# Kernel tuning notes

Measured on AMD Instinct MI355X. Metric: run time of the kernel, lower is better.

Reference implementation:

```python
import jax, jax.numpy as jnp
import numpy as np

NUM_BINS = 16


def _luma(x):
    # x: [B, 3, H, W] -> [B, H, W]
    return 0.299 * x[:, 0] + 0.587 * x[:, 1] + 0.114 * x[:, 2]


def setup_inputs() -> dict:
    key = jax.random.key(0)
    k1, k2, k3 = jax.random.split(key, 3)
    shape = (16, 3, 512, 512)
    pred = jax.random.uniform(k1, shape, dtype=jnp.float32)
    target = jax.random.uniform(k2, shape, dtype=jnp.float32)
    input_img = jax.random.uniform(k3, shape, dtype=jnp.float32)
    return {"pred": pred, "target": target, "input_img": input_img}


def reference(pred, target, input_img):
    nb = NUM_BINS
    pl = _luma(pred).ravel()
    tl = _luma(target).ravel()
    il = _luma(input_img).ravel()
    # bin i covers [i/nb, (i+1)/nb); values >= 1.0 fall in NO bin in the
    # original loop, so route them to an extra segment that is discarded.
    bins = jnp.clip(jnp.floor(il * nb).astype(jnp.int32), 0, nb - 1)
    bins = jnp.where(il >= 1.0, nb, bins)
    ones = jnp.ones_like(il)
    counts = jax.ops.segment_sum(ones, bins, num_segments=nb + 1)[:nb]
    psum = jax.ops.segment_sum(pl, bins, num_segments=nb + 1)[:nb]
    tsum = jax.ops.segment_sum(tl, bins, num_segments=nb + 1)[:nb]
    safe = jnp.maximum(counts, 1.0)
    per_bin = jnp.where(counts > 0, jnp.abs(psum / safe - tsum / safe), 0.0)
    return jnp.sum(per_bin) / nb
```

## Files before the change

### kernel.cpp

```cpp
#include <hip/hip_runtime.h>
#include <hip/hip_bf16.h>


#define CH4 65536
#define NBINS 16
#define NCOL 32

__device__ __forceinline__ float luma_exact(float r, float g, float b) {
    return __fadd_rn(__fadd_rn(__fmul_rn(0.299f, r), __fmul_rn(0.587f, g)),
                     __fmul_rn(0.114f, b));
}

__global__ __launch_bounds__(256) void tm_stage1(
    const float4* __restrict__ pred, const float4* __restrict__ target,
    const float4* __restrict__ input,
    float* __restrict__ partials,
    int G, int rows)
{
    __shared__ float red[4][NCOL];
    const int t = threadIdx.x;
    const int lane = t & 63;
    const int wid = t >> 6;

    float ds[NBINS];
    int cnt[NBINS];
    #pragma unroll
    for (int b = 0; b < NBINS; ++b) { ds[b] = 0.0f; cnt[b] = 0; }

    const int T = gridDim.x * 256;
    for (int g = blockIdx.x * 256 + t; g < G; g += T) {
        const int a = (g >> 16) * (3 * CH4) + (g & (CH4 - 1));
        const float4 i0 = input[a],  i1 = input[a + CH4],  i2 = input[a + 2 * CH4];
        const float4 p0 = pred[a],   p1 = pred[a + CH4],   p2 = pred[a + 2 * CH4];
        const float4 t0 = target[a], t1 = target[a + CH4], t2 = target[a + 2 * CH4];
        const float ir[4] = {i0.x, i0.y, i0.z, i0.w};
        const float ig[4] = {i1.x, i1.y, i1.z, i1.w};
        const float ib[4] = {i2.x, i2.y, i2.z, i2.w};
        const float pr[4] = {p0.x, p0.y, p0.z, p0.w};
        const float pg[4] = {p1.x, p1.y, p1.z, p1.w};
        const float pb[4] = {p2.x, p2.y, p2.z, p2.w};
        const float tr[4] = {t0.x, t0.y, t0.z, t0.w};
        const float tg[4] = {t1.x, t1.y, t1.z, t1.w};
        const float tb[4] = {t2.x, t2.y, t2.z, t2.w};

        #pragma unroll
        for (int j = 0; j < 4; ++j) {
            const float il = luma_exact(ir[j], ig[j], ib[j]);
            int bin = (int)floorf(__fmul_rn(il, 16.0f));
            bin = min(max(bin, 0), NBINS - 1);
            if (il >= 1.0f) bin = NBINS;
            const float d = luma_exact(pr[j], pg[j], pb[j])
                          - luma_exact(tr[j], tg[j], tb[j]);
            #pragma unroll
            for (int b = 0; b < NBINS; ++b) {
                const bool m = (bin == b);
                cnt[b] += (int)__popcll(__ballot(m));
                ds[b]  += m ? d : 0.0f;
            }
        }
    }

    #pragma unroll
    for (int b = 0; b < NBINS; ++b) {
        float v = ds[b];
        v += __shfl_down(v, 32);
        v += __shfl_down(v, 16);
        v += __shfl_down(v, 8);
        v += __shfl_down(v, 4);
        v += __shfl_down(v, 2);
        v += __shfl_down(v, 1);
        if (lane == 0) {
            red[wid][b] = (float)cnt[b];
            red[wid][NBINS + b] = v;
        }
    }
    __syncthreads();
    if (t < NCOL) {
        const float s = red[0][t] + red[1][t] + red[2][t] + red[3][t];
        partials[t * rows + blockIdx.x] = s;
    }
}

__global__ __launch_bounds__(512) void tm_stage2(
    const float4* __restrict__ partials4,
    float* __restrict__ out, int rows4)
{
    __shared__ double col[NCOL];
    const int t = threadIdx.x;
    const int c = t >> 4;
    const int l = t & 15;

    double s = 0.0;
    for (int k = l; k < rows4; k += 16) {
        const float4 v = partials4[c * rows4 + k];
        s += (double)v.x + (double)v.y + (double)v.z + (double)v.w;
    }
    #pragma unroll
    for (int k = 8; k; k >>= 1) s += __shfl_down(s, k, 16);
    if (l == 0) col[c] = s;
    __syncthreads();

    if (t == 0) {
        double acc = 0.0;
        #pragma unroll
        for (int i = 0; i < NBINS; ++i) {
            const double cnt = col[i];
            if (cnt > 0.0) acc += fabs(col[NBINS + i]) / cnt;
        }
        out[0] = (float)(acc / (double)NBINS);
    }
}

extern "C" void kernel_launch(void* const* d_in, const int* in_sizes, int n_in,
                              void* d_out, int out_size, void* d_ws, size_t ws_size,
                              hipStream_t stream) {
    const float* pred   = (const float*)d_in[0];
    const float* target = (const float*)d_in[1];
    const float* input  = (const float*)d_in[2];

    const int G = in_sizes[0] / 12;

    int blocks = 2048;
    const size_t maxRows = ws_size / (NCOL * sizeof(float));
    if ((size_t)blocks > maxRows) blocks = (int)maxRows;
    if (blocks < 1) blocks = 1;
    const int rows = (blocks + 3) & ~3;
    float* partials = (float*)d_ws;

    tm_stage1<<<blocks, 256, 0, stream>>>(
        (const float4*)pred, (const float4*)target, (const float4*)input,
        partials, G, rows);
    tm_stage2<<<1, 512, 0, stream>>>(
        (const float4*)partials, (float*)d_out, rows / 4);
}
```

Measured before the change: 46.83 us.

## Replace ballot-based binning with per-thread LDS histograms and packed byte counters

Replaces the per-pixel 16-way ballot/popcount and select loop with a direct per-thread shared-memory accumulation indexed by bin, plus bin counts packed into two 64-bit byte counters. Each thread processes two pixel groups per iteration and uses nontemporal vector loads, reordering loads so input is consumed before pred/target arrive. The block reduction is rewritten to sum per-bin columns from shared memory. Packed 8-bit counters rely on each thread seeing fewer than 256 pixels per bin, which holds for the current grid size but limits generality.

```diff
diff --git a/kernel.cpp b/kernel.cpp
--- a/kernel.cpp
+++ b/kernel.cpp
@@ -6,78 +6,121 @@
 #define NBINS 16
 #define NCOL 32
 
+typedef float f4 __attribute__((ext_vector_type(4)));
+
 __device__ __forceinline__ float luma_exact(float r, float g, float b) {
     return __fadd_rn(__fadd_rn(__fmul_rn(0.299f, r), __fmul_rn(0.587f, g)),
                      __fmul_rn(0.114f, b));
 }
 
 __global__ __launch_bounds__(256) void tm_stage1(
-    const float4* __restrict__ pred, const float4* __restrict__ target,
-    const float4* __restrict__ input,
+    const f4* __restrict__ pred, const f4* __restrict__ target,
+    const f4* __restrict__ input,
     float* __restrict__ partials,
     int G, int rows)
 {
-    __shared__ float red[4][NCOL];
+    __shared__ float dsh[NBINS * 256];
+    __shared__ unsigned long long cl[256], ch[256];
     const int t = threadIdx.x;
-    const int lane = t & 63;
-    const int wid = t >> 6;
 
-    float ds[NBINS];
-    int cnt[NBINS];
     #pragma unroll
-    for (int b = 0; b < NBINS; ++b) { ds[b] = 0.0f; cnt[b] = 0; }
+    for (int k = 0; k < NBINS; ++k) dsh[k * 256 + t] = 0.0f;
+    __syncthreads();
+
+    unsigned long long cLo = 0ULL, cHi = 0ULL;
 
     const int T = gridDim.x * 256;
-    for (int g = blockIdx.x * 256 + t; g < G; g += T) {
-        const int a = (g >> 16) * (3 * CH4) + (g & (CH4 - 1));
-        const float4 i0 = input[a],  i1 = input[a + CH4],  i2 = input[a + 2 * CH4];
-        const float4 p0 = pred[a],   p1 = pred[a + CH4],   p2 = pred[a + 2 * CH4];
-        const float4 t0 = target[a], t1 = target[a + CH4], t2 = target[a + 2 * CH4];
-        const float ir[4] = {i0.x, i0.y, i0.z, i0.w};
-        const float ig[4] = {i1.x, i1.y, i1.z, i1.w};
-        const float ib[4] = {i2.x, i2.y, i2.z, i2.w};
-        const float pr[4] = {p0.x, p0.y, p0.z, p0.w};
-        const float pg[4] = {p1.x, p1.y, p1.z, p1.w};
-        const float pb[4] = {p2.x, p2.y, p2.z, p2.w};
-        const float tr[4] = {t0.x, t0.y, t0.z, t0.w};
-        const float tg[4] = {t1.x, t1.y, t1.z, t1.w};
-        const float tb[4] = {t2.x, t2.y, t2.z, t2.w};
+    for (int g0 = blockIdx.x * 256 + t; g0 < G; g0 += 2 * T) {
+        const int g1 = g0 + T;
+        const bool ok1 = (g1 < G);
+        const int a0 = (g0 >> 16) * (3 * CH4) + (g0 & (CH4 - 1));
+        const int a1 = ok1 ? (g1 >> 16) * (3 * CH4) + (g1 & (CH4 - 1)) : a0;
+
+        const f4 iA0 = __builtin_nontemporal_load(&input[a0]);
+        const f4 iA1 = __builtin_nontemporal_load(&input[a0 + CH4]);
+        const f4 iA2 = __builtin_nontemporal_load(&input[a0 + 2 * CH4]);
+        const f4 iB0 = __builtin_nontemporal_load(&input[a1]);
+        const f4 iB1 = __builtin_nontemporal_load(&input[a1 + CH4]);
+        const f4 iB2 = __builtin_nontemporal_load(&input[a1 + 2 * CH4]);
+
+        unsigned bpack = 0u, excl = ok1 ? 0u : 0xF0u;
+        #pragma unroll
+        for (int j = 0; j < 4; ++j) {
+            const float ilA = luma_exact(iA0[j], iA1[j], iA2[j]);
+            int bA = (int)floorf(__fmul_rn(ilA, 16.0f));
+            bA = min(max(bA, 0), NBINS - 1);
+            bpack |= (unsigned)bA << (4 * j);
+            excl |= (ilA >= 1.0f ? 1u : 0u) << j;
+
+            const float ilB = luma_exact(iB0[j], iB1[j], iB2[j]);
+            int bB = (int)floorf(__fmul_rn(ilB, 16.0f));
+            bB = min(max(bB, 0), NBINS - 1);
+            bpack |= (unsigned)bB << (4 * (j + 4));
+            excl |= (ilB >= 1.0f ? 1u : 0u) << (j + 4);
+        }
+
+        const f4 pA0 = __builtin_nontemporal_load(&pred[a0]);
+        const f4 pA1 = __builtin_nontemporal_load(&pred[a0 + CH4]);
+        const f4 pA2 = __builtin_nontemporal_load(&pred[a0 + 2 * CH4]);
+        const f4 pB0 = __builtin_nontemporal_load(&pred[a1]);
+        const f4 pB1 = __builtin_nontemporal_load(&pred[a1 + CH4]);
+        const f4 pB2 = __builtin_nontemporal_load(&pred[a1 + 2 * CH4]);
+        float pl[8];
+        #pragma unroll
+        for (int j = 0; j < 4; ++j) {
+            pl[j]     = luma_exact(pA0[j], pA1[j], pA2[j]);
+            pl[j + 4] = luma_exact(pB0[j], pB1[j], pB2[j]);
+        }
+
+        const f4 tA0 = __builtin_nontemporal_load(&target[a0]);
+        const f4 tA1 = __builtin_nontemporal_load(&target[a0 + CH4]);
+        const f4 tA2 = __builtin_nontemporal_load(&target[a0 + 2 * CH4]);
+        const f4 tB0 = __builtin_nontemporal_load(&target[a1]);
+        const f4 tB1 = __builtin_nontemporal_load(&target[a1 + CH4]);
+        const f4 tB2 = __builtin_nontemporal_load(&target[a1 + 2 * CH4]);
 
         #pragma unroll
         for (int j = 0; j < 4; ++j) {
-            const float il = luma_exact(ir[j], ig[j], ib[j]);
-            int bin = (int)floorf(__fmul_rn(il, 16.0f));
-            bin = min(max(bin, 0), NBINS - 1);
-            if (il >= 1.0f) bin = NBINS;
-            const float d = luma_exact(pr[j], pg[j], pb[j])
-                          - luma_exact(tr[j], tg[j], tb[j]);
-            #pragma unroll
-            for (int b = 0; b < NBINS; ++b) {
-                const bool m = (bin == b);
-                cnt[b] += (int)__popcll(__ballot(m));
-                ds[b]  += m ? d : 0.0f;
+            {
+                const float tlA = luma_exact(tA0[j], tA1[j], tA2[j]);
+                if (!((excl >> j) & 1u)) {
+                    const int b = (int)((bpack >> (4 * j)) & 0xFu);
+                    dsh[b * 256 + t] += pl[j] - tlA;
+                    const unsigned long long inc = 1ULL << ((b & 7) * 8);
+                    if (b < 8) cLo += inc; else cHi += inc;
+                }
+            }
+            {
+                const float tlB = luma_exact(tB0[j], tB1[j], tB2[j]);
+                if (!((excl >> (j + 4)) & 1u)) {
+                    const int b = (int)((bpack >> (4 * (j + 4))) & 0xFu);
+                    dsh[b * 256 + t] += pl[j + 4] - tlB;
+                    const unsigned long long inc = 1ULL << ((b & 7) * 8);
+                    if (b < 8) cLo += inc; else cHi += inc;
+                }
             }
         }
     }
 
+    cl[t] = cLo; ch[t] = cHi;
+    __syncthreads();
+
+    const int b = t >> 4, l = t & 15;
+    float s = 0.0f; int c = 0;
     #pragma unroll
-    for (int b = 0; b < NBINS; ++b) {
-        float v = ds[b];
-        v += __shfl_down(v, 32);
-        v += __shfl_down(v, 16);
-        v += __shfl_down(v, 8);
-        v += __shfl_down(v, 4);
-        v += __shfl_down(v, 2);
-        v += __shfl_down(v, 1);
-        if (lane == 0) {
-            red[wid][b] = (float)cnt[b];
-            red[wid][NBINS + b] = v;
-        }
+    for (int k = 0; k < 16; ++k) {
+        s += dsh[b * 256 + k * 16 + l];
+        const unsigned long long packed = (b < 8) ? cl[k * 16 + l] : ch[k * 16 + l];
+        c += (int)((packed >> ((b & 7) * 8)) & 0xFFULL);
     }
-    __syncthreads();
-    if (t < NCOL) {
-        const float s = red[0][t] + red[1][t] + red[2][t] + red[3][t];
-        partials[t * rows + blockIdx.x] = s;
+    #pragma unroll
+    for (int k = 8; k; k >>= 1) {
+        s += __shfl_down(s, k, 16);
+        c += __shfl_down(c, k, 16);
+    }
+    if (l == 0) {
+        partials[b * rows + blockIdx.x] = (float)c;
+        partials[(NBINS + b) * rows + blockIdx.x] = s;
     }
 }
 
@@ -128,7 +171,7 @@
     float* partials = (float*)d_ws;
 
     tm_stage1<<<blocks, 256, 0, stream>>>(
-        (const float4*)pred, (const float4*)target, (const float4*)input,
+        (const f4*)pred, (const f4*)target, (const f4*)input,
         partials, G, rows);
     tm_stage2<<<1, 512, 0, stream>>>(
         (const float4*)partials, (float*)d_out, rows / 4);
```

New measurement: 41.48 us. 11.4% less time.
